# Optimization experiments

Hardware: AMD Instinct MI355X
Metric: run time of the kernel (lower is better)

## Reference

```python
import jax, jax.numpy as jnp
import numpy as np
import math

N_HEADS = 12
D_MODEL = 768
D_HEAD = 64
IGNORE = -100000.0
INIT_STD = 0.02


def setup_inputs() -> dict:
    key = jax.random.key(0)
    ks = jax.random.split(key, 8)
    b, s = 4, 1024
    return {
        "normalized_resid_pre": jax.random.normal(ks[0], (b, 1, s, D_MODEL), jnp.float32),
        "alt_normalized_resid_pre": jax.random.normal(ks[1], (b, s, D_MODEL), jnp.float32),
        "W_Q": jax.random.normal(ks[2], (N_HEADS, D_MODEL, D_HEAD), jnp.float32) * INIT_STD,
        "b_Q": jnp.zeros((N_HEADS, D_HEAD), jnp.float32),
        "W_K": jax.random.normal(ks[3], (N_HEADS, D_MODEL, D_HEAD), jnp.float32) * INIT_STD,
        "b_K": jnp.zeros((N_HEADS, D_HEAD), jnp.float32),
        "W_V": jax.random.normal(ks[4], (N_HEADS, D_MODEL, D_HEAD), jnp.float32) * INIT_STD,
        "b_V": jnp.zeros((N_HEADS, D_HEAD), jnp.float32),
        "W_O": jax.random.normal(ks[5], (N_HEADS, D_HEAD, D_MODEL), jnp.float32) * INIT_STD,
        "b_O": jnp.zeros((D_MODEL,), jnp.float32),
    }


def _apply_attention(x, W_Q, b_Q, W_K, b_K, W_V, b_V, W_O):
    # x: [batch, n_prev(=2), seq, d_model]
    q = jnp.einsum('bpsd,ndh->bpsnh', x, W_Q) + b_Q
    k = jnp.einsum('bpsd,ndh->bpsnh', x, W_K) + b_K
    v = jnp.einsum('bpsd,ndh->bpsnh', x, W_V) + b_V
    scores = jnp.einsum('bpqnh,bpknh->bpnqk', q, k) / math.sqrt(D_HEAD)
    s = scores.shape[-1]
    causal = jnp.triu(jnp.ones((s, s), bool), k=1)  # True above diagonal
    scores = jnp.where(causal, IGNORE, scores)
    pattern = jax.nn.softmax(scores, axis=-1)
    z = jnp.einsum('bpnqk,bpknh->bpqnh', pattern, v)
    # per-head output, NOT summed over heads: [b, p, q, n, d_model]
    return jnp.einsum('bpqnh,nhd->bpqnd', z, W_O)


def reference(normalized_resid_pre, alt_normalized_resid_pre,
              W_Q, b_Q, W_K, b_K, W_V, b_V, W_O, b_O):
    x = jnp.concatenate(
        [normalized_resid_pre, alt_normalized_resid_pre[:, None]], axis=1)  # [b,2,s,d]
    attn_out = _apply_attention(x, W_Q, b_Q, W_K, b_K, W_V, b_V, W_O)  # [b,2,s,n,d]
    old_ablated = attn_out.sum(axis=-2)  # [b,2,s,d]
    orig = attn_out[:, 1]  # [b,s,n,d]
    alt = attn_out[:, 0]   # [b,s,n,d]
    ablate = jnp.ones((N_HEADS, N_HEADS), attn_out.dtype) - jnp.eye(N_HEADS, dtype=attn_out.dtype)
    new_ablated = jnp.einsum('bqnd,kn->bkqd', orig, ablate) + jnp.transpose(alt, (0, 2, 1, 3))
    return jnp.concatenate([old_ablated, new_ablated], axis=1) + b_O  # [b, 2+n_heads, s, d]
```

## Files before the change

kernel.cpp:

```cpp
#include <hip/hip_runtime.h>
#include <math.h>

#define NH 12
#define DM 768
#define DH 64
#define SS 1024

typedef __attribute__((ext_vector_type(8))) short short8;
typedef __attribute__((ext_vector_type(4))) float floatx4;
typedef __attribute__((ext_vector_type(4))) unsigned short usv4;

__device__ __forceinline__ ushort f2bf(float f) {
    union { float f; unsigned u; } v; v.f = f;
    unsigned r = v.u + 0x7fffu + ((v.u >> 16) & 1u);
    return (ushort)(r >> 16);
}
__device__ __forceinline__ float bf2f(ushort u) {
    union { unsigned u; float f; } v; v.u = ((unsigned)u) << 16;
    return v.f;
}

__device__ __forceinline__ void gld_lds16(const ushort* g, ushort* l) {
    __builtin_amdgcn_global_load_lds(
        (const __attribute__((address_space(1))) unsigned int*)g,
        (__attribute__((address_space(3))) unsigned int*)l, 16, 0, 0);
}


__global__ __launch_bounds__(256) void prep_k(
    const float* __restrict__ x0, const float* __restrict__ x1,
    const float* __restrict__ WQ, const float* __restrict__ WK, const float* __restrict__ WV,
    const float* __restrict__ WO,
    ushort* __restrict__ xb, ushort* __restrict__ WbT, ushort* __restrict__ WObT)
{
    __shared__ float T[64][68];
    const int bid = blockIdx.x;
    const int tid = threadIdx.x;
    if (bid < 3072) {
        const size_t e = ((size_t)bid * 256 + tid) * 8;
        const int m = (int)(e / DM), col = (int)(e % DM);
        const int p = (m >> 10) & 1, b = m >> 11, s = m & 1023;
        const float* src = ((p == 0) ? x0 : x1) + (size_t)b * (SS * DM) + (size_t)s * DM + col;
        float4 v0 = *(const float4*)(src);
        float4 v1 = *(const float4*)(src + 4);
        short8 o;
        o[0] = (short)f2bf(v0.x); o[1] = (short)f2bf(v0.y); o[2] = (short)f2bf(v0.z); o[3] = (short)f2bf(v0.w);
        o[4] = (short)f2bf(v1.x); o[5] = (short)f2bf(v1.y); o[6] = (short)f2bf(v1.z); o[7] = (short)f2bf(v1.w);
        *(short8*)(xb + e) = o;
        return;
    }
    const int di = tid >> 2, cg = tid & 3;
    if (bid < 3072 + 432) {
        const int idx = bid - 3072;
        const int tn = idx % 36, dt = idx / 36;
        const int t = tn / NH, n = tn % NH;
        const float* W = ((t == 0) ? WQ : (t == 1) ? WK : WV) + (size_t)n * (DM * DH);
        const int d0 = dt * 64;
#pragma unroll
        for (int j = 0; j < 4; j++) {
            const int c = cg * 16 + j * 4;
            float4 v = *(const float4*)(W + (size_t)(d0 + di) * DH + c);
            *(float4*)&T[di][c] = v;
        }
        __syncthreads();
        ushort* dst = WbT + (size_t)t * (NH * DH * DM) + (size_t)n * (DH * DM) + (size_t)di * DM + d0;
#pragma unroll
        for (int j = 0; j < 4; j++) {
            const int dc = cg * 16 + j * 4;
            usv4 o;
            o[0] = f2bf(T[dc + 0][di]); o[1] = f2bf(T[dc + 1][di]);
            o[2] = f2bf(T[dc + 2][di]); o[3] = f2bf(T[dc + 3][di]);
            *(usv4*)(dst + dc) = o;
        }
        return;
    }
    {
        const int idx = bid - 3072 - 432;
        const int kt = idx % 12, dt = idx / 12;
#pragma unroll
        for (int j = 0; j < 4; j++) {
            const int c = cg * 16 + j * 4;
            float4 v = *(const float4*)(WO + (size_t)(kt * 64 + di) * DM + dt * 64 + c);
            *(float4*)&T[di][c] = v;
        }
        __syncthreads();
        ushort* dst = WObT + (size_t)(dt * 64 + di) * DM + kt * 64;
#pragma unroll
        for (int j = 0; j < 4; j++) {
            const int dc = cg * 16 + j * 4;
            usv4 o;
            o[0] = f2bf(T[dc + 0][di]); o[1] = f2bf(T[dc + 1][di]);
            o[2] = f2bf(T[dc + 2][di]); o[3] = f2bf(T[dc + 3][di]);
            *(usv4*)(dst + dc) = o;
        }
    }
}

__global__ __launch_bounds__(256) void qkv_mfma_k(
    const ushort* __restrict__ xb, const ushort* __restrict__ WbT,
    const float* __restrict__ bQ, const float* __restrict__ bK, const float* __restrict__ bV,
    ushort* __restrict__ Qb, ushort* __restrict__ Kb, ushort* __restrict__ Vtb)
{
    __shared__ ushort As[128 * 32];
    __shared__ ushort Bs[128 * 32];
    const int tid = threadIdx.x;
    const int w = tid >> 6, lane = tid & 63;
    const int l16 = lane & 15, quad = lane >> 4;
    const int jt = blockIdx.x;
    const int mt = blockIdx.y;
    const int t = jt / 6;
    const int jb = (jt % 6) * 128;
    const int mbase = mt * 128;

    const ushort* Bt = WbT + (size_t)t * (DM * DM) + (size_t)jb * DM;

    const int srow = (lane >> 2);
    const int scol = (lane & 3) * 8;
    const ushort* gA0 = xb + (size_t)(mbase + w * 32 + srow) * DM + scol;
    const ushort* gB0 = Bt + (size_t)(w * 32 + srow) * DM + scol;
    ushort* lA0 = As + (w * 32) * 32;
    ushort* lB0 = Bs + (w * 32) * 32;

    floatx4 acc[2][8];
#pragma unroll
    for (int m = 0; m < 2; m++)
#pragma unroll
        for (int n = 0; n < 8; n++) acc[m][n] = (floatx4){0.f, 0.f, 0.f, 0.f};

    for (int kt = 0; kt < 24; kt++) {
        const int k0 = kt * 32;
        __syncthreads();
        gld_lds16(gA0 + k0, lA0);
        gld_lds16(gA0 + (size_t)16 * DM + k0, lA0 + 16 * 32);
        gld_lds16(gB0 + k0, lB0);
        gld_lds16(gB0 + (size_t)16 * DM + k0, lB0 + 16 * 32);
        asm volatile("s_waitcnt vmcnt(0)" ::: "memory");
        __syncthreads();

        const ushort* Ab = As + (w * 32 + l16) * 32 + quad * 8;
        short8 a0 = *(const short8*)(Ab);
        short8 a1 = *(const short8*)(Ab + 16 * 32);
#pragma unroll
        for (int n = 0; n < 8; n++) {
            short8 b = *(const short8*)(Bs + (n * 16 + l16) * 32 + quad * 8);
            acc[0][n] = __builtin_amdgcn_mfma_f32_16x16x32_bf16(a0, b, acc[0][n], 0, 0, 0);
            acc[1][n] = __builtin_amdgcn_mfma_f32_16x16x32_bf16(a1, b, acc[1][n], 0, 0, 0);
        }
    }

    const float* bias = (t == 0) ? bQ : (t == 1) ? bK : bV;
#pragma unroll
    for (int m = 0; m < 2; m++) {
        const int mrow0 = mbase + w * 32 + m * 16 + quad * 4;
        const int bp = mrow0 >> 10;
        const int s0 = mrow0 & 1023;
#pragma unroll
        for (int n = 0; n < 8; n++) {
            const int col = jb + n * 16 + l16;
            const int head = col >> 6, h = col & 63;
            const size_t hb = ((size_t)bp * NH + head) * (SS * DH);
            const float bv = bias[head * DH + h];
            if (t == 0) {
#pragma unroll
                for (int r = 0; r < 4; r++)
                    Qb[hb + (size_t)(s0 + r) * DH + h] = f2bf((acc[m][n][r] + bv) * 0.125f);
            } else if (t == 1) {
#pragma unroll
                for (int r = 0; r < 4; r++)
                    Kb[hb + (size_t)(s0 + r) * DH + h] = f2bf(acc[m][n][r] + bv);
            } else {
                usv4 o;
#pragma unroll
                for (int r = 0; r < 4; r++) o[r] = f2bf(acc[m][n][r] + bv);
                *(usv4*)(Vtb + hb + (size_t)h * SS + s0) = o;
            }
        }
    }
}

__global__ __launch_bounds__(256) void attn_mfma_k(
    const ushort* __restrict__ Qb, const ushort* __restrict__ Kb,
    const ushort* __restrict__ Vtb, ushort* __restrict__ Zb)
{
    __shared__ __align__(16) ushort P_lds[4][16][72];
    const int head = blockIdx.x;
    const int wave = threadIdx.x >> 6;
    const int lane = threadIdx.x & 63;
    const int quad = lane >> 4;
    const int l16  = lane & 15;

    const size_t hb = (size_t)head * (SS * DH);
    const ushort* Qh = Qb + hb;
    const ushort* Kh = Kb + hb;
    const ushort* Vh = Vtb + hb;

#pragma unroll 1
    for (int half = 0; half < 2; half++) {
        const int qtile = (half == 0) ? (15 - (int)blockIdx.y) : (int)blockIdx.y;
        const int qbase = qtile * 64 + wave * 16;
        const int q_lane = qbase + l16;

        short8 b_q0 = *(const short8*)(Qh + (size_t)(qbase + l16) * DH + quad * 8);
        short8 b_q1 = *(const short8*)(Qh + (size_t)(qbase + l16) * DH + 32 + quad * 8);

        floatx4 o[4];
        float m_run = -1e30f, l_run = 0.f;
#pragma unroll
        for (int hg = 0; hg < 4; hg++) o[hg] = (floatx4){0.f, 0.f, 0.f, 0.f};

        const int kb_last = (qbase + 15) >> 6;
        for (int kb = 0; kb <= kb_last; kb++) {
            short8 bv0[4], bv1[4];
#pragma unroll
            for (int hg = 0; hg < 4; hg++) {
                const ushort* vrow = Vh + (size_t)(hg * 16 + l16) * SS + kb * 64 + quad * 8;
                bv0[hg] = *(const short8*)(vrow);
                bv1[hg] = *(const short8*)(vrow + 32);
            }

            floatx4 c[4];
#pragma unroll
            for (int kg = 0; kg < 4; kg++) {
                const ushort* krow = Kh + (size_t)(kb * 64 + kg * 16 + l16) * DH + quad * 8;
                short8 k0 = *(const short8*)(krow);
                short8 k1 = *(const short8*)(krow + 32);
                floatx4 cc = (floatx4){0.f, 0.f, 0.f, 0.f};
                cc = __builtin_amdgcn_mfma_f32_16x16x32_bf16(k0, b_q0, cc, 0, 0, 0);
                cc = __builtin_amdgcn_mfma_f32_16x16x32_bf16(k1, b_q1, cc, 0, 0, 0);
                c[kg] = cc;
            }
            if (kb == kb_last) {
#pragma unroll
                for (int kg = 0; kg < 4; kg++)
#pragma unroll
                    for (int r = 0; r < 4; r++) {
                        const int key = kb * 64 + kg * 16 + quad * 4 + r;
                        if (key > q_lane) c[kg][r] = -1e30f;
                    }
            }

            float mk0 = fmaxf(fmaxf(c[0][0], c[0][1]), fmaxf(c[0][2], c[0][3]));
            float mk1 = fmaxf(fmaxf(c[1][0], c[1][1]), fmaxf(c[1][2], c[1][3]));
            float mk2 = fmaxf(fmaxf(c[2][0], c[2][1]), fmaxf(c[2][2], c[2][3]));
            float mk3 = fmaxf(fmaxf(c[3][0], c[3][1]), fmaxf(c[3][2], c[3][3]));
            float mt = fmaxf(fmaxf(mk0, mk1), fmaxf(mk2, mk3));
            mt = fmaxf(mt, __shfl_xor(mt, 16, 64));
            mt = fmaxf(mt, __shfl_xor(mt, 32, 64));
            const float m_new = fmaxf(m_run, mt);
            const float alpha = __expf(m_run - m_new);
            m_run = m_new;

            float rs = 0.f;
#pragma unroll
            for (int kg = 0; kg < 4; kg++) {
                const float p0 = __expf(c[kg][0] - m_new);
                const float p1 = __expf(c[kg][1] - m_new);
                const float p2 = __expf(c[kg][2] - m_new);
                const float p3 = __expf(c[kg][3] - m_new);
                rs += (p0 + p1) + (p2 + p3);
                const unsigned w0 = ((unsigned)f2bf(p1) << 16) | (unsigned)f2bf(p0);
                const unsigned w1 = ((unsigned)f2bf(p3) << 16) | (unsigned)f2bf(p2);
                *(unsigned*)&P_lds[wave][l16][kg * 16 + quad * 4]     = w0;
                *(unsigned*)&P_lds[wave][l16][kg * 16 + quad * 4 + 2] = w1;
            }
            rs += __shfl_xor(rs, 16, 64);
            rs += __shfl_xor(rs, 32, 64);
            l_run = l_run * alpha + rs;

            float a_o[4];
#pragma unroll
            for (int r = 0; r < 4; r++) a_o[r] = __shfl(alpha, quad * 4 + r, 64);
#pragma unroll
            for (int hg = 0; hg < 4; hg++)
#pragma unroll
                for (int r = 0; r < 4; r++) o[hg][r] *= a_o[r];

            asm volatile("s_waitcnt lgkmcnt(0)" ::: "memory");
            short8 ap0 = *(const short8*)&P_lds[wave][l16][quad * 8];
            short8 ap1 = *(const short8*)&P_lds[wave][l16][32 + quad * 8];
#pragma unroll
            for (int hg = 0; hg < 4; hg++) {
                o[hg] = __builtin_amdgcn_mfma_f32_16x16x32_bf16(ap0, bv0[hg], o[hg], 0, 0, 0);
                o[hg] = __builtin_amdgcn_mfma_f32_16x16x32_bf16(ap1, bv1[hg], o[hg], 0, 0, 0);
            }
            asm volatile("s_waitcnt lgkmcnt(0)" ::: "memory");
        }

        const float inv = 1.f / l_run;
        float inv_o[4];
#pragma unroll
        for (int r = 0; r < 4; r++) inv_o[r] = __shfl(inv, quad * 4 + r, 64);
#pragma unroll
        for (int hg = 0; hg < 4; hg++)
#pragma unroll
            for (int r = 0; r < 4; r++)
                Zb[hb + (size_t)(qbase + quad * 4 + r) * DH + hg * 16 + l16] = f2bf(o[hg][r] * inv_o[r]);
    }
}

__global__ __launch_bounds__(256) void zdiff_k(
    const ushort* __restrict__ Zb, ushort* __restrict__ Zd)
{
    const size_t e = ((size_t)blockIdx.x * 256 + threadIdx.x) * 8;
    const int bk = (int)(e >> 16);
    const int off = (int)(e & 65535);
    const int b_ = bk / NH, k = bk % NH;
    const ushort* z0 = Zb + ((size_t)(b_ * 2) * NH + k) * (SS * DH) + off;
    const ushort* z1 = Zb + ((size_t)(b_ * 2 + 1) * NH + k) * (SS * DH) + off;
    short8 a = *(const short8*)z0;
    short8 c = *(const short8*)z1;
    short8 o;
#pragma unroll
    for (int i = 0; i < 8; i++)
        o[i] = (short)f2bf(bf2f((ushort)a[i]) - bf2f((ushort)c[i]));
    *(short8*)(Zd + e) = o;
}

__global__ __launch_bounds__(256) void outproj_k(
    const ushort* __restrict__ Zb, const ushort* __restrict__ Zd,
    const ushort* __restrict__ WObT, const float* __restrict__ bO,
    float* __restrict__ out)
{
    __shared__ ushort As[64 * 32];
    __shared__ ushort Bs[128 * 32];
    const int tid = threadIdx.x;
    const int w = tid >> 6, lane = tid & 63;
    const int l16 = lane & 15, quad = lane >> 4;
    const int jb = blockIdx.x * 128;
    const int q0 = blockIdx.y * 64;
    const int b_ = blockIdx.z;

    const int srow = lane >> 2;
    const int scol = (lane & 3) * 8;
    const int arow = q0 + w * 16 + srow;
    const ushort* gB = WObT + (size_t)(jb + w * 32 + srow) * DM + scol;
    ushort* lA = As + (w * 16) * 32;
    ushort* lB0 = Bs + (w * 32) * 32;
    ushort* lB1 = Bs + (w * 32 + 16) * 32;

    const ushort* Afrag = As + (w * 16 + l16) * 32 + quad * 8;

    float bia[8];
#pragma unroll
    for (int n = 0; n < 8; n++) bia[n] = bO[jb + n * 16 + l16];

    floatx4 s1[8];
#pragma unroll 1
    for (int pp = 0; pp < 2; pp++) {
        const ushort* Zp = Zb + (size_t)(b_ * 2 + pp) * (NH * SS * DH);
        floatx4 acc[8];
#pragma unroll
        for (int n = 0; n < 8; n++) acc[n] = (floatx4){0.f, 0.f, 0.f, 0.f};
        for (int kt = 0; kt < 24; kt++) {
            const int k0 = kt * 32;
            __syncthreads();
            gld_lds16(Zp + (size_t)(k0 >> 6) * (SS * DH) + (size_t)arow * DH + (k0 & 63) + scol, lA);
            gld_lds16(gB + k0, lB0);
            gld_lds16(gB + (size_t)16 * DM + k0, lB1);
            asm volatile("s_waitcnt vmcnt(0)" ::: "memory");
            __syncthreads();
            short8 a = *(const short8*)(Afrag);
#pragma unroll
            for (int n = 0; n < 8; n++) {
                short8 b = *(const short8*)(Bs + (n * 16 + l16) * 32 + quad * 8);
                acc[n] = __builtin_amdgcn_mfma_f32_16x16x32_bf16(a, b, acc[n], 0, 0, 0);
            }
        }
        float* obase = out + ((size_t)(b_ * 14 + pp) * SS) * DM;
        const int qr = q0 + w * 16 + quad * 4;
#pragma unroll
        for (int n = 0; n < 8; n++) {
            const int d = jb + n * 16 + l16;
#pragma unroll
            for (int r = 0; r < 4; r++) {
                const float v = acc[n][r] + bia[n];
                obase[(size_t)(qr + r) * DM + d] = v;
                if (pp == 1) s1[n][r] = v;
            }
        }
    }

    const ushort* Zdb = Zd + (size_t)b_ * (NH * SS * DH);
#pragma unroll 1
    for (int k = 0; k < NH; k++) {
        const ushort* Zdk = Zdb + (size_t)k * (SS * DH);
        floatx4 acc[8];
#pragma unroll
        for (int n = 0; n < 8; n++) acc[n] = (floatx4){0.f, 0.f, 0.f, 0.f};
#pragma unroll
        for (int kt = 0; kt < 2; kt++) {
            const int k0 = kt * 32;
            __syncthreads();
            gld_lds16(Zdk + (size_t)arow * DH + k0 + scol, lA);
            gld_lds16(gB + k * DH + k0, lB0);
            gld_lds16(gB + (size_t)16 * DM + k * DH + k0, lB1);
            asm volatile("s_waitcnt vmcnt(0)" ::: "memory");
            __syncthreads();
            short8 a = *(const short8*)(Afrag);
#pragma unroll
            for (int n = 0; n < 8; n++) {
                short8 b = *(const short8*)(Bs + (n * 16 + l16) * 32 + quad * 8);
                acc[n] = __builtin_amdgcn_mfma_f32_16x16x32_bf16(a, b, acc[n], 0, 0, 0);
            }
        }
        float* obase = out + ((size_t)(b_ * 14 + 2 + k) * SS) * DM;
        const int qr = q0 + w * 16 + quad * 4;
#pragma unroll
        for (int n = 0; n < 8; n++) {
            const int d = jb + n * 16 + l16;
#pragma unroll
            for (int r = 0; r < 4; r++)
                obase[(size_t)(qr + r) * DM + d] = acc[n][r] + s1[n][r];
        }
    }
}

extern "C" void kernel_launch(void* const* d_in, const int* in_sizes, int n_in,
                              void* d_out, int out_size, void* d_ws, size_t ws_size,
                              hipStream_t stream)
{
    const float* x0 = (const float*)d_in[0];
    const float* x1 = (const float*)d_in[1];
    const float* WQ = (const float*)d_in[2];
    const float* bQ = (const float*)d_in[3];
    const float* WK = (const float*)d_in[4];
    const float* bK = (const float*)d_in[5];
    const float* WV = (const float*)d_in[6];
    const float* bV = (const float*)d_in[7];
    const float* WO = (const float*)d_in[8];
    const float* bO = (const float*)d_in[9];
    float* out = (float*)d_out;

    ushort* ub   = (ushort*)d_ws;
    ushort* Qb   = ub;
    ushort* Kb   = Qb + 6291456;
    ushort* Vtb  = Kb + 6291456;
    ushort* xb   = Vtb + 6291456;
    ushort* WbT  = xb + 6291456;
    ushort* Zb   = WbT + 1769472;
    ushort* WObT = Zb + 6291456;
    ushort* Zd   = WObT + 589824;

    prep_k<<<dim3(3648), 256, 0, stream>>>(x0, x1, WQ, WK, WV, WO, xb, WbT, WObT);
    qkv_mfma_k<<<dim3(18, 64), 256, 0, stream>>>(xb, WbT, bQ, bK, bV, Qb, Kb, Vtb);
    attn_mfma_k<<<dim3(96, 8), 256, 0, stream>>>(Qb, Kb, Vtb, Zb);
    zdiff_k<<<dim3(1536), 256, 0, stream>>>(Zb, Zd);
    outproj_k<<<dim3(6, 16, 4), 256, 0, stream>>>(Zb, Zd, WObT, bO, out);
}
```

Baseline: 411.9 us.

## Stage K/V tiles in swizzled LDS shared across waves; remap block-to-head order

Each attention block now loads each 64-key K tile and V^T tile once into XOR-swizzled shared memory with direct global-to-LDS loads. The four waves then read their MFMA operands from LDS instead of each wave fetching the same K/V data from global memory. The grid is flattened and remapped so that consecutive blocks cover 8 heads sharing a query-pair index, which may improve L2 locality. In exchange, the loop adds two barriers per key block and waits on vmcnt(0), so global-load latency is no longer overlapped with compute. Waves with earlier queries also now run up to the full qtile key range, with masking handling the extra keys.

```diff
diff --git a/kernel.cpp b/kernel.cpp
--- a/kernel.cpp
+++ b/kernel.cpp
@@ -182,8 +182,13 @@
     const ushort* __restrict__ Qb, const ushort* __restrict__ Kb,
     const ushort* __restrict__ Vtb, ushort* __restrict__ Zb)
 {
+    __shared__ __align__(16) ushort Ks[64 * 64];
+    __shared__ __align__(16) ushort Vs[64 * 64];
     __shared__ __align__(16) ushort P_lds[4][16][72];
-    const int head = blockIdx.x;
+
+    const int bid  = blockIdx.x;
+    const int head = (bid & 7) + ((bid >> 6) << 3);
+    const int qpair = (bid >> 3) & 7;
     const int wave = threadIdx.x >> 6;
     const int lane = threadIdx.x & 63;
     const int quad = lane >> 4;
@@ -194,9 +199,12 @@
     const ushort* Kh = Kb + hb;
     const ushort* Vh = Vtb + hb;
 
+    const int srl = lane >> 3;
+    const int su  = lane & 7;
+
 #pragma unroll 1
     for (int half = 0; half < 2; half++) {
-        const int qtile = (half == 0) ? (15 - (int)blockIdx.y) : (int)blockIdx.y;
+        const int qtile = (half == 0) ? (15 - qpair) : qpair;
         const int qbase = qtile * 64 + wave * 16;
         const int q_lane = qbase + l16;
 
@@ -208,22 +216,28 @@
 #pragma unroll
         for (int hg = 0; hg < 4; hg++) o[hg] = (floatx4){0.f, 0.f, 0.f, 0.f};
 
-        const int kb_last = (qbase + 15) >> 6;
+        const int kb_last = qtile;
         for (int kb = 0; kb <= kb_last; kb++) {
-            short8 bv0[4], bv1[4];
-#pragma unroll
-            for (int hg = 0; hg < 4; hg++) {
-                const ushort* vrow = Vh + (size_t)(hg * 16 + l16) * SS + kb * 64 + quad * 8;
-                bv0[hg] = *(const short8*)(vrow);
-                bv1[hg] = *(const short8*)(vrow + 32);
-            }
+            __syncthreads();
+#pragma unroll
+            for (int j = 0; j < 2; j++) {
+                const int rl  = j * 8 + srl;
+                const int row = wave * 16 + rl;
+                const int uu  = su ^ (rl & 7);
+                gld_lds16(Kh + (size_t)(kb * 64 + row) * DH + uu * 8,
+                          Ks + wave * 1024 + j * 512);
+                gld_lds16(Vh + (size_t)row * SS + kb * 64 + uu * 8,
+                          Vs + wave * 1024 + j * 512);
+            }
+            asm volatile("s_waitcnt vmcnt(0)" ::: "memory");
+            __syncthreads();
 
             floatx4 c[4];
 #pragma unroll
             for (int kg = 0; kg < 4; kg++) {
-                const ushort* krow = Kh + (size_t)(kb * 64 + kg * 16 + l16) * DH + quad * 8;
-                short8 k0 = *(const short8*)(krow);
-                short8 k1 = *(const short8*)(krow + 32);
+                const int r = kg * 16 + l16;
+                short8 k0 = *(const short8*)(Ks + r * 64 + ((quad ^ (r & 7)) * 8));
+                short8 k1 = *(const short8*)(Ks + r * 64 + (((quad + 4) ^ (r & 7)) * 8));
                 floatx4 cc = (floatx4){0.f, 0.f, 0.f, 0.f};
                 cc = __builtin_amdgcn_mfma_f32_16x16x32_bf16(k0, b_q0, cc, 0, 0, 0);
                 cc = __builtin_amdgcn_mfma_f32_16x16x32_bf16(k1, b_q1, cc, 0, 0, 0);
@@ -280,8 +294,11 @@
             short8 ap1 = *(const short8*)&P_lds[wave][l16][32 + quad * 8];
 #pragma unroll
             for (int hg = 0; hg < 4; hg++) {
-                o[hg] = __builtin_amdgcn_mfma_f32_16x16x32_bf16(ap0, bv0[hg], o[hg], 0, 0, 0);
-                o[hg] = __builtin_amdgcn_mfma_f32_16x16x32_bf16(ap1, bv1[hg], o[hg], 0, 0, 0);
+                const int h = hg * 16 + l16;
+                short8 bv0 = *(const short8*)(Vs + h * 64 + ((quad ^ (h & 7)) * 8));
+                short8 bv1 = *(const short8*)(Vs + h * 64 + (((quad + 4) ^ (h & 7)) * 8));
+                o[hg] = __builtin_amdgcn_mfma_f32_16x16x32_bf16(ap0, bv0, o[hg], 0, 0, 0);
+                o[hg] = __builtin_amdgcn_mfma_f32_16x16x32_bf16(ap1, bv1, o[hg], 0, 0, 0);
             }
             asm volatile("s_waitcnt lgkmcnt(0)" ::: "memory");
         }
@@ -443,7 +460,7 @@
 
     prep_k<<<dim3(3648), 256, 0, stream>>>(x0, x1, WQ, WK, WV, WO, xb, WbT, WObT);
     qkv_mfma_k<<<dim3(18, 64), 256, 0, stream>>>(xb, WbT, bQ, bK, bV, Qb, Kb, Vtb);
-    attn_mfma_k<<<dim3(96, 8), 256, 0, stream>>>(Qb, Kb, Vtb, Zb);
+    attn_mfma_k<<<dim3(768), 256, 0, stream>>>(Qb, Kb, Vtb, Zb);
     zdiff_k<<<dim3(1536), 256, 0, stream>>>(Zb, Zd);
     outproj_k<<<dim3(6, 16, 4), 256, 0, stream>>>(Zb, Zd, WObT, bO, out);
 }
```

Measured after the change: 354.1 us. -14.0%, faster.
